# Optimization experiments

Measured on AMD Instinct MI355X. Metric: run time of the kernel, lower is better.

The kernel has to match this reference:

```python
import jax, jax.numpy as jnp
import numpy as np

N_EMBD = 1024
N_HEAD = 16
EPS = 1e-5

def layer_norm(x, g, b):
    mu = jnp.mean(x, axis=-1, keepdims=True)
    var = jnp.mean(jnp.square(x - mu), axis=-1, keepdims=True)
    return (x - mu) * jax.lax.rsqrt(var + EPS) * g + b

def setup_inputs() -> dict:
    key = jax.random.key(0)
    ks = jax.random.split(key, 12)
    C = N_EMBD
    s = lambda n: 1.0 / np.sqrt(n)
    return {
        "x": jax.random.normal(ks[0], (4, 2048, C), dtype=jnp.float32),
        "ln1_g": jnp.ones((C,), jnp.float32),
        "ln1_b": jnp.zeros((C,), jnp.float32),
        "attn_w": jax.random.normal(ks[1], (C, 3 * C), dtype=jnp.float32) * s(C),
        "attn_b": jnp.zeros((3 * C,), jnp.float32),
        "proj_w": jax.random.normal(ks[2], (C, C), dtype=jnp.float32) * s(C),
        "proj_b": jnp.zeros((C,), jnp.float32),
        "ln2_g": jnp.ones((C,), jnp.float32),
        "ln2_b": jnp.zeros((C,), jnp.float32),
        "fc1_w": jax.random.normal(ks[3], (C, 4 * C), dtype=jnp.float32) * s(C),
        "fc1_b": jnp.zeros((4 * C,), jnp.float32),
        "fc2_w": jax.random.normal(ks[4], (4 * C, C), dtype=jnp.float32) * s(4 * C),
        "fc2_b": jnp.zeros((C,), jnp.float32),
    }

def reference(x, ln1_g, ln1_b, attn_w, attn_b, proj_w, proj_b,
              ln2_g, ln2_b, fc1_w, fc1_b, fc2_w, fc2_b):
    B, T, C = x.shape
    H = N_HEAD
    D = C // H

    # --- self attention on ln1(x) ---
    h = layer_norm(x, ln1_g, ln1_b)
    qkv = h @ attn_w + attn_b                       # [B,T,3C]
    q, k, v = jnp.split(qkv, 3, axis=-1)
    q = q.reshape(B, T, H, D).transpose(0, 2, 1, 3)  # [B,H,T,D]
    k = k.reshape(B, T, H, D).transpose(0, 2, 1, 3)
    v = v.reshape(B, T, H, D).transpose(0, 2, 1, 3)
    att = jnp.einsum("bhqd,bhkd->bhqk", q, k) * (D ** -0.5)
    causal = jnp.tril(jnp.ones((T, T), dtype=bool))
    att = jnp.where(causal[None, None], att, -jnp.inf)
    att = jax.nn.softmax(att, axis=-1)
    y = jnp.einsum("bhqk,bhkd->bhqd", att, v)        # [B,H,T,D]
    y = y.transpose(0, 2, 1, 3).reshape(B, T, C)
    y = y @ proj_w + proj_b
    x = x + y

    # --- MLP on ln2(x) ---
    h = layer_norm(x, ln2_g, ln2_b)
    h = jax.nn.relu(h @ fc1_w + fc1_b)
    h = h @ fc2_w + fc2_b
    return x + h
```

## Files before the change

kernel.cpp:

```cpp
#include <hip/hip_runtime.h>
#include <cstdint>
#include <cstddef>

typedef __bf16 bf16x8 __attribute__((ext_vector_type(8)));
typedef float f32x4 __attribute__((ext_vector_type(4)));
typedef float f32x16 __attribute__((ext_vector_type(16)));
typedef unsigned short u16;
typedef unsigned uint2v __attribute__((ext_vector_type(2)));

namespace {
constexpr int Bb = 4, Tt = 2048, Cc = 1024, Hh = 16, Dd = 64;
constexpr int ROWS = Bb * Tt;
constexpr int C3 = 3 * Cc;
constexpr float LNEPS = 1e-5f;
constexpr float SCL2 = 0.18033688011112042f;
}

__device__ __forceinline__ u16 f2bf(float f) {
  union { float f; unsigned u; } v; v.f = f;
  return (u16)((v.u + 0x7fffu + ((v.u >> 16) & 1u)) >> 16);
}
__device__ __forceinline__ u16 bfn(float f) {
  union { __bf16 b; u16 u; } t; t.b = (__bf16)f; return t.u;
}
__device__ __forceinline__ unsigned pk2(float lo, float hi) {
  union { __bf16 b[2]; unsigned u; } t;
  t.b[0] = (__bf16)lo; t.b[1] = (__bf16)hi;
  return t.u;
}
__device__ __forceinline__ float exp2_hw(float x) {
  float r;
  asm("v_exp_f32 %0, %1" : "=v"(r) : "v"(x));
  return r;
}
__device__ __forceinline__ uint2v plswap(unsigned a, unsigned b) {
  return __builtin_amdgcn_permlane32_swap(a, b, false, false);
}
__device__ __forceinline__ float xhalf_max(float x) {
  union { float f; unsigned u; } c; c.f = x;
  uint2v r = plswap(c.u, c.u);
  union { unsigned u; float f; } a, b; a.u = r[0]; b.u = r[1];
  return fmaxf(a.f, b.f);
}
__device__ __forceinline__ float xhalf_sum(float x) {
  union { float f; unsigned u; } c; c.f = x;
  uint2v r = plswap(c.u, c.u);
  union { unsigned u; float f; } a, b; a.u = r[0]; b.u = r[1];
  return a.f + b.f;
}

typedef __attribute__((address_space(3))) unsigned lds_u32;
typedef __attribute__((address_space(1))) const unsigned glb_u32;
__device__ __forceinline__ void gload_lds16(const u16* g, u16* l) {
  __builtin_amdgcn_global_load_lds((glb_u32*)g, (lds_u32*)l, 16, 0, 0);
}

__global__ __launch_bounds__(256) void ln_kernel(
    const float* __restrict__ x, const float* __restrict__ g,
    const float* __restrict__ b, u16* __restrict__ out)
{
  const int row = blockIdx.x;
  const int tid = threadIdx.x;
  const float4 v = reinterpret_cast<const float4*>(x + (size_t)row * Cc)[tid];
  float s  = v.x + v.y + v.z + v.w;
  float ss = v.x * v.x + v.y * v.y + v.z * v.z + v.w * v.w;
#pragma unroll
  for (int off = 32; off; off >>= 1) {
    s  += __shfl_xor(s, off);
    ss += __shfl_xor(ss, off);
  }
  __shared__ float sa[4], sb[4];
  const int w = tid >> 6;
  if ((tid & 63) == 0) { sa[w] = s; sb[w] = ss; }
  __syncthreads();
  s  = sa[0] + sa[1] + sa[2] + sa[3];
  ss = sb[0] + sb[1] + sb[2] + sb[3];
  const float mu   = s * (1.0f / Cc);
  const float var  = ss * (1.0f / Cc) - mu * mu;
  const float rstd = rsqrtf(var + LNEPS);
  const float4 gv = reinterpret_cast<const float4*>(g)[tid];
  const float4 bv = reinterpret_cast<const float4*>(b)[tid];
  ushort4 o;
  o.x = f2bf((v.x - mu) * rstd * gv.x + bv.x);
  o.y = f2bf((v.y - mu) * rstd * gv.y + bv.y);
  o.z = f2bf((v.z - mu) * rstd * gv.z + bv.z);
  o.w = f2bf((v.w - mu) * rstd * gv.w + bv.w);
  reinterpret_cast<ushort4*>(out + (size_t)row * Cc)[tid] = o;
}

__global__ __launch_bounds__(256) void wcast_t(
    const float* __restrict__ w, u16* __restrict__ wt, int K, int N)
{
  __shared__ float tile[32][33];
  const int n0 = blockIdx.x * 32, k0 = blockIdx.y * 32;
  const int tx = threadIdx.x & 31, ty = threadIdx.x >> 5;
#pragma unroll
  for (int i = 0; i < 4; i++)
    tile[ty + i * 8][tx] = w[(size_t)(k0 + ty + i * 8) * N + n0 + tx];
  __syncthreads();
#pragma unroll
  for (int i = 0; i < 4; i++)
    wt[(size_t)(n0 + ty + i * 8) * K + k0 + tx] = f2bf(tile[tx][ty + i * 8]);
}

enum { EPI_BIAS_BF16 = 0, EPI_BIAS_RELU_BF16 = 1, EPI_BIAS_RES_F32 = 2 };

template <int EPI>
__global__ __launch_bounds__(512, 2) void gemm256(
    const u16* __restrict__ A, const u16* __restrict__ Bt,
    const float* __restrict__ bias, const float* __restrict__ res,
    void* __restrict__ outp, int M, int N, int K)
{
  __shared__ alignas(16) u16 Al[4][256 * 32];
  __shared__ alignas(16) u16 Bl[4][256 * 32];

  const int tid  = threadIdx.x;
  const int lane = tid & 63;
  const int wv   = tid >> 6;
  const int wr   = wv >> 2, wc = wv & 3;
  const int lr   = lane & 15;
  const int lg   = (lane >> 4) & 3;

  const int q8  = (int)gridDim.x >> 3;
  const int lid = ((int)blockIdx.x & 7) * q8 + ((int)blockIdx.x >> 3);
  const int bm = (lid & 31) << 8;
  const int bn = (lid >> 5) << 8;

  const int srl  = tid >> 2;
  const int schk = (tid & 3) ^ ((tid >> 3) & 3);
  const u16* gA = A  + (size_t)(bm + srl) * K + schk * 8;
  const u16* gB = Bt + (size_t)(bn + srl) * K + schk * 8;
  const size_t rowK128 = (size_t)128 * K;

  const int fsw  = (lg ^ ((lr >> 1) & 3)) * 8;
  const int arow = wr * 128 + lr;
  const int brow = wc * 64 + lr;

  f32x4 acc[8][4];
#pragma unroll
  for (int mi = 0; mi < 8; mi++)
#pragma unroll
    for (int nj = 0; nj < 4; nj++)
      acc[mi][nj] = (f32x4){0.f, 0.f, 0.f, 0.f};

  const int NT = K >> 5;

  auto stageA = [&](int t) {
    u16* d = &Al[t & 3][tid * 8];
    gload_lds16(gA + (size_t)t * 32, d);
    gload_lds16(gA + rowK128 + (size_t)t * 32, d + 4096);
  };
  auto stageB = [&](int t) {
    u16* d = &Bl[t & 3][tid * 8];
    gload_lds16(gB + (size_t)t * 32, d);
    gload_lds16(gB + rowK128 + (size_t)t * 32, d + 4096);
  };

  for (int t = 0; t < 3; ++t) { stageA(t); stageB(t); }
  asm volatile("s_waitcnt vmcnt(8)" ::: "memory");
  asm volatile("s_barrier" ::: "memory");

  for (int kt = 0; kt < NT; ++kt) {
    const u16* Ab = &Al[kt & 3][0];
    const u16* Bb = &Bl[kt & 3][0];
    const bool st = (kt + 3 < NT);

    bf16x8 bf[4];
#pragma unroll
    for (int nj = 0; nj < 4; ++nj)
      bf[nj] = *reinterpret_cast<const bf16x8*>(Bb + (brow + nj * 16) * 32 + fsw);
    bf16x8 af[4];
#pragma unroll
    for (int m = 0; m < 4; ++m)
      af[m] = *reinterpret_cast<const bf16x8*>(Ab + (arow + m * 16) * 32 + fsw);
    if (st) stageA(kt + 3);
    asm volatile("s_barrier" ::: "memory");
    __builtin_amdgcn_s_setprio(1);
#pragma unroll
    for (int m = 0; m < 4; ++m)
#pragma unroll
      for (int nj = 0; nj < 4; ++nj)
        acc[m][nj] = __builtin_amdgcn_mfma_f32_16x16x32_bf16(af[m], bf[nj], acc[m][nj], 0, 0, 0);
    __builtin_amdgcn_s_setprio(0);
    asm volatile("s_barrier" ::: "memory");

#pragma unroll
    for (int m = 0; m < 4; ++m)
      af[m] = *reinterpret_cast<const bf16x8*>(Ab + (arow + (m + 4) * 16) * 32 + fsw);
    if (st) stageB(kt + 3);
    if (kt < NT - 3)       { asm volatile("s_waitcnt vmcnt(8)" ::: "memory"); }
    else if (kt == NT - 3) { asm volatile("s_waitcnt vmcnt(4)" ::: "memory"); }
    else if (kt == NT - 2) { asm volatile("s_waitcnt vmcnt(0)" ::: "memory"); }
    asm volatile("s_barrier" ::: "memory");
    __builtin_amdgcn_s_setprio(1);
#pragma unroll
    for (int m = 0; m < 4; ++m)
#pragma unroll
      for (int nj = 0; nj < 4; ++nj)
        acc[m + 4][nj] = __builtin_amdgcn_mfma_f32_16x16x32_bf16(af[m], bf[nj], acc[m + 4][nj], 0, 0, 0);
    __builtin_amdgcn_s_setprio(0);
    asm volatile("s_barrier" ::: "memory");
  }

#pragma unroll
  for (int mi = 0; mi < 8; ++mi) {
    const int row0 = bm + wr * 128 + mi * 16 + lg * 4;
#pragma unroll
    for (int nj = 0; nj < 4; ++nj) {
      const int col = bn + wc * 64 + nj * 16 + lr;
      const float bv = bias[col];
#pragma unroll
      for (int r = 0; r < 4; ++r) {
        const int row = row0 + r;
        float v = acc[mi][nj][r] + bv;
        if constexpr (EPI == EPI_BIAS_RELU_BF16) v = fmaxf(v, 0.0f);
        if constexpr (EPI == EPI_BIAS_RES_F32) {
          float* out = (float*)outp;
          out[(size_t)row * N + col] = v + res[(size_t)row * N + col];
        } else {
          ((u16*)outp)[(size_t)row * N + col] = f2bf(v);
        }
      }
    }
  }
}

template <int EPI>
__global__ __launch_bounds__(256, 3) void gemm_bt(
    const u16* __restrict__ A, const u16* __restrict__ Bt,
    const float* __restrict__ bias, const float* __restrict__ res,
    void* __restrict__ outp, int M, int N, int K)
{
  constexpr int BM = 128, BN = 128, BK = 64;
  __shared__ alignas(16) u16 As[BM][BK];
  __shared__ alignas(16) u16 Bs[BN][BK];
  const int tid  = threadIdx.x;
  const int lane = tid & 63;
  const int wv   = tid >> 6;
  const int wr   = wv >> 1, wc = wv & 1;
  const int lr   = lane & 15, lg = lane >> 4;

  const int q8  = (int)gridDim.x >> 3;
  const int lid = ((int)blockIdx.x & 7) * q8 + ((int)blockIdx.x >> 3);
  const int bm = (lid & 63) << 7;
  const int bn = (lid >> 6) << 7;

  f32x4 acc[4][4];
#pragma unroll
  for (int mi = 0; mi < 4; mi++)
#pragma unroll
    for (int nj = 0; nj < 4; nj++)
      acc[mi][nj] = (f32x4){0.f, 0.f, 0.f, 0.f};

  const int srow = tid >> 3;
  const int scol = (tid & 7) * 8;
  const u16* ga = &A [(size_t)(bm + srow) * K + scol];
  const u16* gb = &Bt[(size_t)(bn + srow) * K + scol];
  u16* as_dst = &As[0][0] + (size_t)tid * 8;
  u16* bs_dst = &Bs[0][0] + (size_t)tid * 8;

  for (int k0 = 0; k0 < K; k0 += BK) {
#pragma unroll
    for (int p = 0; p < 4; p++) {
      gload_lds16(ga + (size_t)p * 32 * K + k0, as_dst + p * 2048);
      gload_lds16(gb + (size_t)p * 32 * K + k0, bs_dst + p * 2048);
    }
    __syncthreads();
#pragma unroll
    for (int kk = 0; kk < BK; kk += 32) {
      bf16x8 af[4], bfr[4];
#pragma unroll
      for (int mi = 0; mi < 4; mi++)
        af[mi] = *reinterpret_cast<const bf16x8*>(&As[wr * 64 + mi * 16 + lr][kk + lg * 8]);
#pragma unroll
      for (int nj = 0; nj < 4; nj++)
        bfr[nj] = *reinterpret_cast<const bf16x8*>(&Bs[wc * 64 + nj * 16 + lr][kk + lg * 8]);
#pragma unroll
      for (int mi = 0; mi < 4; mi++)
#pragma unroll
        for (int nj = 0; nj < 4; nj++)
          acc[mi][nj] = __builtin_amdgcn_mfma_f32_16x16x32_bf16(af[mi], bfr[nj], acc[mi][nj], 0, 0, 0);
    }
    __syncthreads();
  }

#pragma unroll
  for (int mi = 0; mi < 4; mi++) {
#pragma unroll
    for (int nj = 0; nj < 4; nj++) {
      const int col = bn + wc * 64 + nj * 16 + lr;
      const float bv = bias[col];
#pragma unroll
      for (int r = 0; r < 4; r++) {
        const int row = bm + wr * 64 + mi * 16 + lg * 4 + r;
        float v = acc[mi][nj][r] + bv;
        if constexpr (EPI == EPI_BIAS_RELU_BF16) v = fmaxf(v, 0.0f);
        if constexpr (EPI == EPI_BIAS_RES_F32) {
          float* out = (float*)outp;
          out[(size_t)row * N + col] = v + res[(size_t)row * N + col];
        } else {
          ((u16*)outp)[(size_t)row * N + col] = f2bf(v);
        }
      }
    }
  }
}

__global__ __launch_bounds__(256) void build_vt(
    const u16* __restrict__ qkv, u16* __restrict__ vt)
{
  __shared__ u16 tile[64][80];
  const int t0 = blockIdx.x * 64;
  const int h  = blockIdx.y;
  const int b  = blockIdx.z;
  const int tid = threadIdx.x;
  const int rr = tid >> 3, cc = (tid & 7) * 8;
#pragma unroll
  for (int p = 0; p < 2; p++) {
    const int t = rr + p * 32;
    bf16x8 v = *reinterpret_cast<const bf16x8*>(
        &qkv[(size_t)(b * Tt + t0 + t) * C3 + 2 * Cc + h * Dd + cc]);
    *reinterpret_cast<bf16x8*>(&tile[t][cc]) = v;
  }
  __syncthreads();
#pragma unroll
  for (int p = 0; p < 2; p++) {
    const int d = rr + p * 32;
    union { u16 u[8]; int4 v; } o;
#pragma unroll
    for (int j = 0; j < 8; j++) o.u[j] = tile[cc + j][d];
    *reinterpret_cast<int4*>(&vt[(size_t)((b * Hh + h) * Dd + d) * Tt + t0 + cc]) = o.v;
  }
}

__global__ __launch_bounds__(512, 2) void flash_attn(
    const u16* __restrict__ qkv,
    const u16* __restrict__ vt,
    u16* __restrict__ y)
{
  const int tid = threadIdx.x, lane = tid & 63, wv = tid >> 6;
  const int l31 = lane & 31, hf = lane >> 5;

  const int bid = blockIdx.x;
  const int lid = (bid & 7) * 32 + (bid >> 3);
  const int bh = lid >> 2, pg = lid & 3;
  const int b = bh >> 4, h = bh & 15;
  const int sbase = pg * 4 + (wv & 3);
  const int s = (wv < 4) ? sbase : (31 - sbase);

  const u16* qbase = qkv + (size_t)b * Tt * C3 + h * Dd;
  const u16* kbase = qbase + Cc;
  const u16* vbase = vt + (size_t)bh * Dd * Tt;

  bool dmask[16];
#pragma unroll
  for (int r = 0; r < 16; r++)
    dmask[r] = ((r & 3) + 8 * (r >> 2) + 4 * hf) > l31;

  const int qa0 = s * 64;
  const int qb0 = qa0 + 32;
  const int ta = 2 * s;

  bf16x8 qfa[4], qfb[4];
#pragma unroll
  for (int kc = 0; kc < 4; kc++) {
    qfa[kc] = *reinterpret_cast<const bf16x8*>(
        &qbase[(size_t)(qa0 + l31) * C3 + kc * 16 + hf * 8]);
    qfb[kc] = *reinterpret_cast<const bf16x8*>(
        &qbase[(size_t)(qb0 + l31) * C3 + kc * 16 + hf * 8]);
  }

  f32x16 oa[2], ob[2];
#pragma unroll
  for (int i = 0; i < 16; i++) { oa[0][i] = 0.f; oa[1][i] = 0.f; ob[0][i] = 0.f; ob[1][i] = 0.f; }
  float mA = -INFINITY, lA = 0.0f, mB = -INFINITY, lB = 0.0f;

  const u16* kptr = &kbase[(size_t)l31 * C3 + hf * 8];
  const u16* vp0 = &vbase[(size_t)l31 * Tt + hf * 8];
  const u16* vp1 = vp0 + (size_t)32 * Tt;

  bf16x8 kf[4];
#pragma unroll
  for (int kc = 0; kc < 4; kc++)
    kf[kc] = *reinterpret_cast<const bf16x8*>(kptr + kc * 16);

  for (int kt = 0; kt <= ta; ++kt) {
    bf16x8 vf[2][2];
#pragma unroll
    for (int ch = 0; ch < 2; ch++) {
      vf[0][ch] = *reinterpret_cast<const bf16x8*>(vp0 + ch * 16);
      vf[1][ch] = *reinterpret_cast<const bf16x8*>(vp1 + ch * 16);
    }
    vp0 += 32; vp1 += 32;

    f32x16 sA, sB;
#pragma unroll
    for (int i = 0; i < 16; i++) { sA[i] = 0.f; sB[i] = 0.f; }
#pragma unroll
    for (int kc = 0; kc < 4; kc++) {
      sA = __builtin_amdgcn_mfma_f32_32x32x16_bf16(kf[kc], qfa[kc], sA, 0, 0, 0);
      sB = __builtin_amdgcn_mfma_f32_32x32x16_bf16(kf[kc], qfb[kc], sB, 0, 0, 0);
    }

    kptr += (size_t)32 * C3;
    bf16x8 kn[4];
#pragma unroll
    for (int kc = 0; kc < 4; kc++)
      kn[kc] = *reinterpret_cast<const bf16x8*>(kptr + kc * 16);

    const bool diagA = (kt == ta);

    float svA[16], svB[16];
#pragma unroll
    for (int r = 0; r < 16; r++) {
      svA[r] = sA[r];
      if (diagA && dmask[r]) svA[r] = -INFINITY;
      svB[r] = sB[r];
    }

    float mAa = fmaxf(fmaxf(svA[0], svA[1]), fmaxf(svA[2], svA[3]));
    float mAb = fmaxf(fmaxf(svA[4], svA[5]), fmaxf(svA[6], svA[7]));
    float mAc = fmaxf(fmaxf(svA[8], svA[9]), fmaxf(svA[10], svA[11]));
    float mAd = fmaxf(fmaxf(svA[12], svA[13]), fmaxf(svA[14], svA[15]));
    float m8A = fmaxf(fmaxf(mAa, mAb), fmaxf(mAc, mAd));
    float mBa = fmaxf(fmaxf(svB[0], svB[1]), fmaxf(svB[2], svB[3]));
    float mBb = fmaxf(fmaxf(svB[4], svB[5]), fmaxf(svB[6], svB[7]));
    float mBc = fmaxf(fmaxf(svB[8], svB[9]), fmaxf(svB[10], svB[11]));
    float mBd = fmaxf(fmaxf(svB[12], svB[13]), fmaxf(svB[14], svB[15]));
    float m8B = fmaxf(fmaxf(mBa, mBb), fmaxf(mBc, mBd));
    m8A = xhalf_max(m8A);
    m8B = xhalf_max(m8B);

    if (!__all(m8A - mA <= 64.0f)) {
      const float mnew  = fmaxf(mA, m8A);
      const float alpha = exp2_hw((mA - mnew) * SCL2);
      lA *= alpha;
#pragma unroll
      for (int i = 0; i < 16; i++) { oa[0][i] *= alpha; oa[1][i] *= alpha; }
      mA = mnew;
    }
    if (!__all(m8B - mB <= 64.0f)) {
      const float mnew  = fmaxf(mB, m8B);
      const float alpha = exp2_hw((mB - mnew) * SCL2);
      lB *= alpha;
#pragma unroll
      for (int i = 0; i < 16; i++) { ob[0][i] *= alpha; ob[1][i] *= alpha; }
      mB = mnew;
    }

    const float msA = mA * SCL2;
    const float msB = mB * SCL2;
    float pA[16], pB[16];
#pragma unroll
    for (int r = 0; r < 16; r++) {
      pA[r] = exp2_hw(fmaf(svA[r], SCL2, -msA));
      pB[r] = exp2_hw(fmaf(svB[r], SCL2, -msB));
    }
    {
      float a0 = ((pA[0] + pA[1]) + (pA[2] + pA[3])) + ((pA[4] + pA[5]) + (pA[6] + pA[7]));
      float a1 = ((pA[8] + pA[9]) + (pA[10] + pA[11])) + ((pA[12] + pA[13]) + (pA[14] + pA[15]));
      lA += a0 + a1;
      float b0 = ((pB[0] + pB[1]) + (pB[2] + pB[3])) + ((pB[4] + pB[5]) + (pB[6] + pB[7]));
      float b1 = ((pB[8] + pB[9]) + (pB[10] + pB[11])) + ((pB[12] + pB[13]) + (pB[14] + pB[15]));
      lB += b0 + b1;
    }

    unsigned pwA[2][4], pwB[2][4];
#pragma unroll
    for (int ch = 0; ch < 2; ch++) {
      const int bs = ch * 8;
      {
        unsigned w0 = pk2(pA[bs + 0], pA[bs + 1]);
        unsigned w1 = pk2(pA[bs + 2], pA[bs + 3]);
        unsigned w2 = pk2(pA[bs + 4], pA[bs + 5]);
        unsigned w3 = pk2(pA[bs + 6], pA[bs + 7]);
        uint2v r02 = plswap(w0, w2);
        uint2v r13 = plswap(w1, w3);
        pwA[ch][0] = r02[0]; pwA[ch][2] = r02[1];
        pwA[ch][1] = r13[0]; pwA[ch][3] = r13[1];
      }
      {
        unsigned w0 = pk2(pB[bs + 0], pB[bs + 1]);
        unsigned w1 = pk2(pB[bs + 2], pB[bs + 3]);
        unsigned w2 = pk2(pB[bs + 4], pB[bs + 5]);
        unsigned w3 = pk2(pB[bs + 6], pB[bs + 7]);
        uint2v r02 = plswap(w0, w2);
        uint2v r13 = plswap(w1, w3);
        pwB[ch][0] = r02[0]; pwB[ch][2] = r02[1];
        pwB[ch][1] = r13[0]; pwB[ch][3] = r13[1];
      }
    }

#pragma unroll
    for (int d0i = 0; d0i < 2; d0i++)
#pragma unroll
      for (int ch = 0; ch < 2; ch++) {
        union { unsigned w[4]; bf16x8 v; } pa, pb;
        pa.w[0] = pwA[ch][0]; pa.w[1] = pwA[ch][1];
        pa.w[2] = pwA[ch][2]; pa.w[3] = pwA[ch][3];
        pb.w[0] = pwB[ch][0]; pb.w[1] = pwB[ch][1];
        pb.w[2] = pwB[ch][2]; pb.w[3] = pwB[ch][3];
        oa[d0i] = __builtin_amdgcn_mfma_f32_32x32x16_bf16(vf[d0i][ch], pa.v, oa[d0i], 0, 0, 0);
        ob[d0i] = __builtin_amdgcn_mfma_f32_32x32x16_bf16(vf[d0i][ch], pb.v, ob[d0i], 0, 0, 0);
      }

#pragma unroll
    for (int kc = 0; kc < 4; kc++) kf[kc] = kn[kc];
  }

  {
    bf16x8 vf[2][2];
#pragma unroll
    for (int ch = 0; ch < 2; ch++) {
      vf[0][ch] = *reinterpret_cast<const bf16x8*>(vp0 + ch * 16);
      vf[1][ch] = *reinterpret_cast<const bf16x8*>(vp1 + ch * 16);
    }

    f32x16 sB;
#pragma unroll
    for (int i = 0; i < 16; i++) sB[i] = 0.f;
#pragma unroll
    for (int kc = 0; kc < 4; kc++)
      sB = __builtin_amdgcn_mfma_f32_32x32x16_bf16(kf[kc], qfb[kc], sB, 0, 0, 0);

    float svB[16];
#pragma unroll
    for (int r = 0; r < 16; r++) {
      svB[r] = sB[r];
      if (dmask[r]) svB[r] = -INFINITY;
    }
    float mBa = fmaxf(fmaxf(svB[0], svB[1]), fmaxf(svB[2], svB[3]));
    float mBb = fmaxf(fmaxf(svB[4], svB[5]), fmaxf(svB[6], svB[7]));
    float mBc = fmaxf(fmaxf(svB[8], svB[9]), fmaxf(svB[10], svB[11]));
    float mBd = fmaxf(fmaxf(svB[12], svB[13]), fmaxf(svB[14], svB[15]));
    float m8B = fmaxf(fmaxf(mBa, mBb), fmaxf(mBc, mBd));
    m8B = xhalf_max(m8B);

    if (!__all(m8B - mB <= 64.0f)) {
      const float mnew  = fmaxf(mB, m8B);
      const float alpha = exp2_hw((mB - mnew) * SCL2);
      lB *= alpha;
#pragma unroll
      for (int i = 0; i < 16; i++) { ob[0][i] *= alpha; ob[1][i] *= alpha; }
      mB = mnew;
    }
    const float msB = mB * SCL2;
    float pB[16];
#pragma unroll
    for (int r = 0; r < 16; r++)
      pB[r] = exp2_hw(fmaf(svB[r], SCL2, -msB));
    {
      float b0 = ((pB[0] + pB[1]) + (pB[2] + pB[3])) + ((pB[4] + pB[5]) + (pB[6] + pB[7]));
      float b1 = ((pB[8] + pB[9]) + (pB[10] + pB[11])) + ((pB[12] + pB[13]) + (pB[14] + pB[15]));
      lB += b0 + b1;
    }
    unsigned pwB[2][4];
#pragma unroll
    for (int ch = 0; ch < 2; ch++) {
      const int bs = ch * 8;
      unsigned w0 = pk2(pB[bs + 0], pB[bs + 1]);
      unsigned w1 = pk2(pB[bs + 2], pB[bs + 3]);
      unsigned w2 = pk2(pB[bs + 4], pB[bs + 5]);
      unsigned w3 = pk2(pB[bs + 6], pB[bs + 7]);
      uint2v r02 = plswap(w0, w2);
      uint2v r13 = plswap(w1, w3);
      pwB[ch][0] = r02[0]; pwB[ch][2] = r02[1];
      pwB[ch][1] = r13[0]; pwB[ch][3] = r13[1];
    }
#pragma unroll
    for (int d0i = 0; d0i < 2; d0i++)
#pragma unroll
      for (int ch = 0; ch < 2; ch++) {
        union { unsigned w[4]; bf16x8 v; } pb;
        pb.w[0] = pwB[ch][0]; pb.w[1] = pwB[ch][1];
        pb.w[2] = pwB[ch][2]; pb.w[3] = pwB[ch][3];
        ob[d0i] = __builtin_amdgcn_mfma_f32_32x32x16_bf16(vf[d0i][ch], pb.v, ob[d0i], 0, 0, 0);
      }
  }

  {
    const float lsA = xhalf_sum(lA);
    const float invA = 1.0f / lsA;
    u16* yrow = y + (size_t)(b * Tt + qa0 + l31) * Cc + h * Dd;
#pragma unroll
    for (int d0i = 0; d0i < 2; d0i++)
#pragma unroll
      for (int qd = 0; qd < 4; qd++) {
        ushort4 o;
        o.x = bfn(oa[d0i][qd * 4 + 0] * invA);
        o.y = bfn(oa[d0i][qd * 4 + 1] * invA);
        o.z = bfn(oa[d0i][qd * 4 + 2] * invA);
        o.w = bfn(oa[d0i][qd * 4 + 3] * invA);
        *reinterpret_cast<ushort4*>(&yrow[d0i * 32 + qd * 8 + hf * 4]) = o;
      }
  }
  {
    const float lsB = xhalf_sum(lB);
    const float invB = 1.0f / lsB;
    u16* yrow = y + (size_t)(b * Tt + qb0 + l31) * Cc + h * Dd;
#pragma unroll
    for (int d0i = 0; d0i < 2; d0i++)
#pragma unroll
      for (int qd = 0; qd < 4; qd++) {
        ushort4 o;
        o.x = bfn(ob[d0i][qd * 4 + 0] * invB);
        o.y = bfn(ob[d0i][qd * 4 + 1] * invB);
        o.z = bfn(ob[d0i][qd * 4 + 2] * invB);
        o.w = bfn(ob[d0i][qd * 4 + 3] * invB);
        *reinterpret_cast<ushort4*>(&yrow[d0i * 32 + qd * 8 + hf * 4]) = o;
      }
  }
}

extern "C" void kernel_launch(void* const* d_in, const int* in_sizes, int n_in,
                              void* d_out, int out_size, void* d_ws, size_t ws_size,
                              hipStream_t stream)
{
  const float* x      = (const float*)d_in[0];
  const float* ln1_g  = (const float*)d_in[1];
  const float* ln1_b  = (const float*)d_in[2];
  const float* attn_w = (const float*)d_in[3];
  const float* attn_b = (const float*)d_in[4];
  const float* proj_w = (const float*)d_in[5];
  const float* proj_b = (const float*)d_in[6];
  const float* ln2_g  = (const float*)d_in[7];
  const float* ln2_b  = (const float*)d_in[8];
  const float* fc1_w  = (const float*)d_in[9];
  const float* fc1_b  = (const float*)d_in[10];
  const float* fc2_w  = (const float*)d_in[11];
  const float* fc2_b  = (const float*)d_in[12];
  float* out = (float*)d_out;

  char* ws = (char*)d_ws;
  size_t o = 0;
  auto alloc = [&](size_t bytes) { char* p = ws + o; o += bytes; return p; };
  u16* wqkv_t  = (u16*)alloc((size_t)C3 * Cc * 2);
  u16* wproj_t = (u16*)alloc((size_t)Cc * Cc * 2);
  u16* wfc1_t  = (u16*)alloc((size_t)4096 * Cc * 2);
  u16* wfc2_t  = (u16*)alloc((size_t)Cc * 4096 * 2);
  u16* h_bf    = (u16*)alloc((size_t)ROWS * Cc * 2);
  u16* y_bf    = (u16*)alloc((size_t)ROWS * Cc * 2);
  u16* qkv_raw = (u16*)alloc((size_t)ROWS * C3 * 2);
  u16* vt      = (u16*)alloc((size_t)Bb * Hh * Dd * Tt * 2);
  u16* hh      = qkv_raw;

  wcast_t<<<dim3(C3 / 32, Cc / 32), 256, 0, stream>>>(attn_w, wqkv_t, Cc, C3);
  wcast_t<<<dim3(Cc / 32, Cc / 32), 256, 0, stream>>>(proj_w, wproj_t, Cc, Cc);
  wcast_t<<<dim3(4096 / 32, Cc / 32), 256, 0, stream>>>(fc1_w, wfc1_t, Cc, 4096);
  wcast_t<<<dim3(Cc / 32, 4096 / 32), 256, 0, stream>>>(fc2_w, wfc2_t, 4096, Cc);

  ln_kernel<<<ROWS, 256, 0, stream>>>(x, ln1_g, ln1_b, h_bf);
  gemm256<EPI_BIAS_BF16><<<32 * (C3 / 256), 512, 0, stream>>>(
      h_bf, wqkv_t, attn_b, nullptr, qkv_raw, ROWS, C3, Cc);
  build_vt<<<dim3(Tt / 64, Hh, Bb), 256, 0, stream>>>(qkv_raw, vt);
  flash_attn<<<dim3(256), 512, 0, stream>>>(qkv_raw, vt, y_bf);
  gemm_bt<EPI_BIAS_RES_F32><<<64 * (Cc / 128), 256, 0, stream>>>(
      y_bf, wproj_t, proj_b, x, out, ROWS, Cc, Cc);
  ln_kernel<<<ROWS, 256, 0, stream>>>(out, ln2_g, ln2_b, h_bf);
  gemm256<EPI_BIAS_RELU_BF16><<<32 * (4096 / 256), 512, 0, stream>>>(
      h_bf, wfc1_t, fc1_b, nullptr, hh, ROWS, 4096, Cc);
  gemm_bt<EPI_BIAS_RES_F32><<<64 * (Cc / 128), 256, 0, stream>>>(
      hh, wfc2_t, fc2_b, out, out, ROWS, Cc, 4096);
}
```

Before: 398.4 us.

## Replace proj/fc2 GEMM with 256x128 tile, 4-stage pipelined, swizzled LDS kernel

Replaces the simple 128x128 single-buffered gemm_bt used for the projection and fc2 GEMMs with a 512-thread 256x128 tile kernel. It stages operands through a 4-deep LDS ring with direct global-to-LDS loads and explicit vmcnt waits, XOR-swizzles the LDS layout, and raises MFMA wave priority. The goal is to hide global load latency and avoid LDS bank conflicts, which the old kernel exposed by syncing on every K step. The trade-offs are fewer blocks (256 for N=1024), more registers and LDS per block, and hand-written barrier/waitcnt logic that is fragile.

Measured after the change: 429.9 us. 7.9% more time.

```diff
diff --git a/kernel.cpp b/kernel.cpp
--- a/kernel.cpp
+++ b/kernel.cpp
@@ -226,73 +226,110 @@
 }
 
 template <int EPI>
-__global__ __launch_bounds__(256, 3) void gemm_bt(
+__global__ __launch_bounds__(512, 2) void gemm256n(
     const u16* __restrict__ A, const u16* __restrict__ Bt,
     const float* __restrict__ bias, const float* __restrict__ res,
     void* __restrict__ outp, int M, int N, int K)
 {
-  constexpr int BM = 128, BN = 128, BK = 64;
-  __shared__ alignas(16) u16 As[BM][BK];
-  __shared__ alignas(16) u16 Bs[BN][BK];
+  __shared__ alignas(16) u16 Al[4][256 * 32];
+  __shared__ alignas(16) u16 Bl[4][128 * 32];
+
   const int tid  = threadIdx.x;
   const int lane = tid & 63;
   const int wv   = tid >> 6;
-  const int wr   = wv >> 1, wc = wv & 1;
-  const int lr   = lane & 15, lg = lane >> 4;
+  const int wr   = wv >> 2, wc = wv & 3;
+  const int lr   = lane & 15;
+  const int lg   = (lane >> 4) & 3;
 
   const int q8  = (int)gridDim.x >> 3;
   const int lid = ((int)blockIdx.x & 7) * q8 + ((int)blockIdx.x >> 3);
-  const int bm = (lid & 63) << 7;
-  const int bn = (lid >> 6) << 7;
-
-  f32x4 acc[4][4];
-#pragma unroll
-  for (int mi = 0; mi < 4; mi++)
-#pragma unroll
-    for (int nj = 0; nj < 4; nj++)
+  const int bm = (lid & 31) << 8;
+  const int bn = (lid >> 5) << 7;
+
+  const int srl  = tid >> 2;
+  const int schk = (tid & 3) ^ ((tid >> 3) & 3);
+  const u16* gA = A  + (size_t)(bm + srl) * K + schk * 8;
+  const u16* gB = Bt + (size_t)(bn + srl) * K + schk * 8;
+  const size_t rowK128 = (size_t)128 * K;
+
+  const int fsw  = (lg ^ ((lr >> 1) & 3)) * 8;
+  const int arow = wr * 128 + lr;
+  const int brow = wc * 32 + lr;
+
+  f32x4 acc[8][2];
+#pragma unroll
+  for (int mi = 0; mi < 8; mi++)
+#pragma unroll
+    for (int nj = 0; nj < 2; nj++)
       acc[mi][nj] = (f32x4){0.f, 0.f, 0.f, 0.f};
 
-  const int srow = tid >> 3;
-  const int scol = (tid & 7) * 8;
-  const u16* ga = &A [(size_t)(bm + srow) * K + scol];
-  const u16* gb = &Bt[(size_t)(bn + srow) * K + scol];
-  u16* as_dst = &As[0][0] + (size_t)tid * 8;
-  u16* bs_dst = &Bs[0][0] + (size_t)tid * 8;
-
-  for (int k0 = 0; k0 < K; k0 += BK) {
-#pragma unroll
-    for (int p = 0; p < 4; p++) {
-      gload_lds16(ga + (size_t)p * 32 * K + k0, as_dst + p * 2048);
-      gload_lds16(gb + (size_t)p * 32 * K + k0, bs_dst + p * 2048);
-    }
-    __syncthreads();
-#pragma unroll
-    for (int kk = 0; kk < BK; kk += 32) {
-      bf16x8 af[4], bfr[4];
-#pragma unroll
-      for (int mi = 0; mi < 4; mi++)
-        af[mi] = *reinterpret_cast<const bf16x8*>(&As[wr * 64 + mi * 16 + lr][kk + lg * 8]);
-#pragma unroll
-      for (int nj = 0; nj < 4; nj++)
-        bfr[nj] = *reinterpret_cast<const bf16x8*>(&Bs[wc * 64 + nj * 16 + lr][kk + lg * 8]);
-#pragma unroll
-      for (int mi = 0; mi < 4; mi++)
-#pragma unroll
-        for (int nj = 0; nj < 4; nj++)
-          acc[mi][nj] = __builtin_amdgcn_mfma_f32_16x16x32_bf16(af[mi], bfr[nj], acc[mi][nj], 0, 0, 0);
-    }
-    __syncthreads();
-  }
-
-#pragma unroll
-  for (int mi = 0; mi < 4; mi++) {
-#pragma unroll
-    for (int nj = 0; nj < 4; nj++) {
-      const int col = bn + wc * 64 + nj * 16 + lr;
+  const int NT = K >> 5;
+
+  auto stageA = [&](int t) {
+    u16* d = &Al[t & 3][tid * 8];
+    gload_lds16(gA + (size_t)t * 32, d);
+    gload_lds16(gA + rowK128 + (size_t)t * 32, d + 4096);
+  };
+  auto stageB = [&](int t) {
+    gload_lds16(gB + (size_t)t * 32, &Bl[t & 3][tid * 8]);
+  };
+
+  for (int t = 0; t < 3; ++t) { stageA(t); stageB(t); }
+  asm volatile("s_waitcnt vmcnt(6)" ::: "memory");
+  asm volatile("s_barrier" ::: "memory");
+
+  for (int kt = 0; kt < NT; ++kt) {
+    const u16* Ab = &Al[kt & 3][0];
+    const u16* Bb = &Bl[kt & 3][0];
+    const bool st = (kt + 3 < NT);
+
+    bf16x8 bf[2];
+#pragma unroll
+    for (int nj = 0; nj < 2; ++nj)
+      bf[nj] = *reinterpret_cast<const bf16x8*>(Bb + (brow + nj * 16) * 32 + fsw);
+    bf16x8 af[4];
+#pragma unroll
+    for (int m = 0; m < 4; ++m)
+      af[m] = *reinterpret_cast<const bf16x8*>(Ab + (arow + m * 16) * 32 + fsw);
+    if (st) stageA(kt + 3);
+    asm volatile("s_barrier" ::: "memory");
+    __builtin_amdgcn_s_setprio(1);
+#pragma unroll
+    for (int m = 0; m < 4; ++m)
+#pragma unroll
+      for (int nj = 0; nj < 2; ++nj)
+        acc[m][nj] = __builtin_amdgcn_mfma_f32_16x16x32_bf16(af[m], bf[nj], acc[m][nj], 0, 0, 0);
+    __builtin_amdgcn_s_setprio(0);
+    asm volatile("s_barrier" ::: "memory");
+
+#pragma unroll
+    for (int m = 0; m < 4; ++m)
+      af[m] = *reinterpret_cast<const bf16x8*>(Ab + (arow + (m + 4) * 16) * 32 + fsw);
+    if (st) stageB(kt + 3);
+    if (kt < NT - 3)       { asm volatile("s_waitcnt vmcnt(6)" ::: "memory"); }
+    else if (kt == NT - 3) { asm volatile("s_waitcnt vmcnt(3)" ::: "memory"); }
+    else if (kt == NT - 2) { asm volatile("s_waitcnt vmcnt(0)" ::: "memory"); }
+    asm volatile("s_barrier" ::: "memory");
+    __builtin_amdgcn_s_setprio(1);
+#pragma unroll
+    for (int m = 0; m < 4; ++m)
+#pragma unroll
+      for (int nj = 0; nj < 2; ++nj)
+        acc[m + 4][nj] = __builtin_amdgcn_mfma_f32_16x16x32_bf16(af[m], bf[nj], acc[m + 4][nj], 0, 0, 0);
+    __builtin_amdgcn_s_setprio(0);
+    asm volatile("s_barrier" ::: "memory");
+  }
+
+#pragma unroll
+  for (int mi = 0; mi < 8; ++mi) {
+    const int row0 = bm + wr * 128 + mi * 16 + lg * 4;
+#pragma unroll
+    for (int nj = 0; nj < 2; ++nj) {
+      const int col = bn + wc * 32 + nj * 16 + lr;
       const float bv = bias[col];
 #pragma unroll
-      for (int r = 0; r < 4; r++) {
-        const int row = bm + wr * 64 + mi * 16 + lg * 4 + r;
+      for (int r = 0; r < 4; ++r) {
+        const int row = row0 + r;
         float v = acc[mi][nj][r] + bv;
         if constexpr (EPI == EPI_BIAS_RELU_BF16) v = fmaxf(v, 0.0f);
         if constexpr (EPI == EPI_BIAS_RES_F32) {
@@ -654,11 +691,11 @@
       h_bf, wqkv_t, attn_b, nullptr, qkv_raw, ROWS, C3, Cc);
   build_vt<<<dim3(Tt / 64, Hh, Bb), 256, 0, stream>>>(qkv_raw, vt);
   flash_attn<<<dim3(256), 512, 0, stream>>>(qkv_raw, vt, y_bf);
-  gemm_bt<EPI_BIAS_RES_F32><<<64 * (Cc / 128), 256, 0, stream>>>(
+  gemm256n<EPI_BIAS_RES_F32><<<32 * (Cc / 128), 512, 0, stream>>>(
       y_bf, wproj_t, proj_b, x, out, ROWS, Cc, Cc);
   ln_kernel<<<ROWS, 256, 0, stream>>>(out, ln2_g, ln2_b, h_bf);
   gemm256<EPI_BIAS_RELU_BF16><<<32 * (4096 / 256), 512, 0, stream>>>(
       h_bf, wfc1_t, fc1_b, nullptr, hh, ROWS, 4096, Cc);
-  gemm_bt<EPI_BIAS_RES_F32><<<64 * (Cc / 128), 256, 0, stream>>>(
+  gemm256n<EPI_BIAS_RES_F32><<<32 * (Cc / 128), 512, 0, stream>>>(
       hh, wfc2_t, fc2_b, out, out, ROWS, Cc, 4096);
 }
```
